# Kernel tuning notes

Measured on AMD Instinct MI355X. Metric: run time of the kernel, lower is better.

## Reference

```python
import jax, jax.numpy as jnp
import numpy as np

EPS = 1e-8

def _layernorm(x, gamma, beta):
    # torch-style: std with Bessel correction (ddof=1), eps added to std
    D = x.shape[-1]
    mean = jnp.mean(x, axis=-1, keepdims=True)
    var = jnp.sum((x - mean) ** 2, axis=-1, keepdims=True) / (D - 1)
    std = jnp.sqrt(var)
    return (x - mean) / (std + EPS) * gamma + beta


def setup_inputs() -> dict:
    key = jax.random.key(0)
    B, T, D, H = 1, 2048, 1024, 16
    Dh = D // H
    ks = jax.random.split(key, 8)
    s = 0.02
    return {
        "x": jax.random.normal(ks[0], (B, T, D), jnp.float32),
        "wq": jax.random.normal(ks[1], (H, D, Dh), jnp.float32) * s,
        "wk": jax.random.normal(ks[2], (H, D, Dh), jnp.float32) * s,
        "wv": jax.random.normal(ks[3], (H, D, Dh), jnp.float32) * s,
        "wo": jax.random.normal(ks[4], (D, D), jnp.float32) * s,
        "bo": jnp.zeros((D,), jnp.float32),
        "ln1_g": jnp.ones((D,), jnp.float32),
        "ln1_b": jnp.zeros((D,), jnp.float32),
        "ln2_g": jnp.ones((D,), jnp.float32),
        "ln2_b": jnp.zeros((D,), jnp.float32),
        "w1": jax.random.normal(ks[5], (D, 4 * D), jnp.float32) * s,
        "b1": jnp.zeros((4 * D,), jnp.float32),
        "w2": jax.random.normal(ks[6], (4 * D, D), jnp.float32) * s,
        "b2": jnp.zeros((D,), jnp.float32),
    }


def reference(x, wq, wk, wv, wo, bo, ln1_g, ln1_b, ln2_g, ln2_b, w1, b1, w2, b2):
    B, T, D = x.shape
    H, _, Dh = wq.shape
    # --- attention sublayer (dropout p used at eval => identity) ---
    h = _layernorm(x, ln1_g, ln1_b)
    q = jnp.einsum('btd,hde->bhte', h, wq)
    k = jnp.einsum('btd,hde->bhte', h, wk)
    v = jnp.einsum('btd,hde->bhte', h, wv)
    scores = jnp.einsum('bhte,bhse->bhts', q, k) / jnp.sqrt(jnp.float32(Dh))
    causal = jnp.triu(jnp.ones((T, T), bool), 1)  # True above diagonal => masked
    scores = jnp.where(causal, -jnp.inf, scores)
    attn = jax.nn.softmax(scores, axis=-1)
    ctx = jnp.einsum('bhts,bhse->bthe', attn, v).reshape(B, T, H * Dh)
    att_out = ctx @ wo + bo
    x = x + att_out
    # --- FFN sublayer ---
    h2 = _layernorm(x, ln2_g, ln2_b)
    ffn = jax.nn.gelu(h2 @ w1 + b1, approximate=False) @ w2 + b2
    return x + ffn
```

## Files before the change

### kernel.cpp

```cpp
#include <hip/hip_runtime.h>
#include <hip/hip_bf16.h>
#include <math.h>

typedef unsigned short bf16u;
typedef __attribute__((ext_vector_type(8))) short short8;
typedef __attribute__((ext_vector_type(4))) float floatx4;

__device__ __forceinline__ float bf2f(bf16u u) {
  union { unsigned int i; float f; } c;
  c.i = ((unsigned int)u) << 16;
  return c.f;
}
__device__ __forceinline__ bf16u f2bf(float f) {
  union { float f; unsigned int i; } c;
  c.f = f;
  unsigned int lsb = (c.i >> 16) & 1u;
  c.i += 0x7fffu + lsb;
  return (bf16u)(c.i >> 16);
}

__device__ __forceinline__ void load_lds16(const void* g, void* l) {
  __builtin_amdgcn_global_load_lds(
      (const __attribute__((address_space(1))) void*)g,
      (__attribute__((address_space(3))) void*)l, 16, 0, 0);
}

__global__ __launch_bounds__(256) void ln_kernel(
    const float* __restrict__ x, bf16u* __restrict__ out,
    const float* __restrict__ gamma, const float* __restrict__ beta) {
  const int row = blockIdx.x;
  const int tid = threadIdx.x;
  const int lane = tid & 63, wave = tid >> 6;
  __shared__ float red[4];
  const float* xr = x + (size_t)row * 1024;
  float v[4];
#pragma unroll
  for (int i = 0; i < 4; i++) v[i] = xr[tid + i * 256];
  float s = v[0] + v[1] + v[2] + v[3];
#pragma unroll
  for (int off = 32; off; off >>= 1) s += __shfl_down(s, off);
  if (lane == 0) red[wave] = s;
  __syncthreads();
  const float mean = (red[0] + red[1] + red[2] + red[3]) * (1.0f / 1024.0f);
  __syncthreads();
  float sq = 0.f;
#pragma unroll
  for (int i = 0; i < 4; i++) { float d = v[i] - mean; sq += d * d; }
#pragma unroll
  for (int off = 32; off; off >>= 1) sq += __shfl_down(sq, off);
  if (lane == 0) red[wave] = sq;
  __syncthreads();
  const float var = (red[0] + red[1] + red[2] + red[3]) * (1.0f / 1023.0f);
  const float inv = 1.0f / (sqrtf(var) + 1e-8f);
  bf16u* orow = out + (size_t)row * 1024;
#pragma unroll
  for (int i = 0; i < 4; i++) {
    int idx = tid + i * 256;
    orow[idx] = f2bf((v[i] - mean) * inv * gamma[idx] + beta[idx]);
  }
}

__global__ __launch_bounds__(256) void pack_weights(
    const float* __restrict__ wq, const float* __restrict__ wk,
    const float* __restrict__ wv, const float* __restrict__ wo,
    const float* __restrict__ w1, const float* __restrict__ w2,
    bf16u* __restrict__ WqkvT, bf16u* __restrict__ woT,
    bf16u* __restrict__ w1T, bf16u* __restrict__ w2T) {
  __shared__ bf16u tile[32][33];
  const int id = blockIdx.x;
  const float* in; bf16u* out; int R, C, bx, by;
  if (id < 3072) {
    int job = id >> 10, rem = id & 1023;
    int head = rem >> 6, t = rem & 63;
    bx = t & 1; by = t >> 1;
    in = (job == 0 ? wq : (job == 1 ? wk : wv)) + head * 65536;
    out = WqkvT + job * 1048576 + head * 65536;
    R = 1024; C = 64;
  } else if (id < 4096) {
    int rem = id - 3072; bx = rem & 31; by = rem >> 5;
    in = wo; out = woT; R = 1024; C = 1024;
  } else if (id < 8192) {
    int rem = id - 4096; bx = rem & 127; by = rem >> 7;
    in = w1; out = w1T; R = 1024; C = 4096;
  } else {
    int rem = id - 8192; bx = rem & 31; by = rem >> 5;
    in = w2; out = w2T; R = 4096; C = 1024;
  }
  const int bc = bx * 32, br = by * 32;
  const int lx = threadIdx.x & 31, ly = threadIdx.x >> 5;
#pragma unroll
  for (int i = 0; i < 32; i += 8)
    tile[ly + i][lx] = f2bf(in[(size_t)(br + ly + i) * C + bc + lx]);
  __syncthreads();
#pragma unroll
  for (int i = 0; i < 32; i += 8)
    out[(size_t)(bc + ly + i) * R + br + lx] = tile[lx][ly + i];
}

__global__ __launch_bounds__(256) void transpose_b(
    const bf16u* __restrict__ in, bf16u* __restrict__ out,
    int ins, int coff, int outs) {
  __shared__ bf16u tile[32][33];
  const int bc = blockIdx.x * 32, br = blockIdx.y * 32;
  const int lx = threadIdx.x & 31, ly = threadIdx.x >> 5;
#pragma unroll
  for (int i = 0; i < 32; i += 8)
    tile[ly + i][lx] = in[(size_t)(br + ly + i) * ins + coff + bc + lx];
  __syncthreads();
#pragma unroll
  for (int i = 0; i < 32; i += 8)
    out[(size_t)(bc + ly + i) * outs + br + lx] = tile[lx][ly + i];
}

template <int BM, int BN, int WGR, int WGC, int EPI>
__global__ __launch_bounds__(256, (BN == 128 ? 2 : 4)) void gemm_bt(
    const bf16u* __restrict__ A, const bf16u* __restrict__ Bt,
    const float* __restrict__ bias, const float* __restrict__ res,
    void* __restrict__ Cout, int M, int N, int K, int kchunk) {
  constexpr int BK = 64;
  constexpr int TM = BM / WGR, TN = BN / WGC;
  constexpr int NI = TM / 16, NJ = TN / 16;
  alignas(16) __shared__ bf16u sA[BM * BK];
  alignas(16) __shared__ bf16u sB[BN * BK];
  const int tid = threadIdx.x, lane = tid & 63, wave = tid >> 6;
  const int wr = wave / WGC, wc = wave % WGC;
  const int quad = lane >> 4, l16 = lane & 15;
  const int m0 = blockIdx.y * BM, n0 = blockIdx.x * BN;
  const int kz = blockIdx.z;
  const int kbeg = kz * kchunk;
  const int kend = (kbeg + kchunk < K) ? (kbeg + kchunk) : K;

  floatx4 acc[NI][NJ] = {};
  constexpr int ACH = BM * BK / 8;
  constexpr int BCH = BN * BK / 8;

  for (int k0 = kbeg; k0 < kend; k0 += BK) {
#pragma unroll
    for (int c = tid; c < ACH; c += 256) {
      int r = c >> 3, kc = ((c ^ r) & 7) * 8;
      load_lds16(A + (size_t)(m0 + r) * K + k0 + kc, (void*)(sA + c * 8));
    }
#pragma unroll
    for (int c = tid; c < BCH; c += 256) {
      int r = c >> 3, kc = ((c ^ r) & 7) * 8;
      load_lds16(Bt + (size_t)(n0 + r) * K + k0 + kc, (void*)(sB + c * 8));
    }
    __syncthreads();
#pragma unroll
    for (int kk = 0; kk < BK; kk += 32) {
      const int ch = (kk >> 3) + quad;
      short8 af[NI], bf[NJ];
#pragma unroll
      for (int i = 0; i < NI; i++) {
        const int R = wr * TM + i * 16 + l16;
        af[i] = *(const short8*)(sA + R * BK + ((ch ^ (R & 7)) << 3));
      }
#pragma unroll
      for (int j = 0; j < NJ; j++) {
        const int R = wc * TN + j * 16 + l16;
        bf[j] = *(const short8*)(sB + R * BK + ((ch ^ (R & 7)) << 3));
      }
#pragma unroll
      for (int i = 0; i < NI; i++)
#pragma unroll
        for (int j = 0; j < NJ; j++)
          acc[i][j] = __builtin_amdgcn_mfma_f32_16x16x32_bf16(af[i], bf[j], acc[i][j], 0, 0, 0);
    }
    __syncthreads();
  }

  float* pout = (float*)Cout;
  if constexpr (EPI == 3) pout += (size_t)kz * M * N;
#pragma unroll
  for (int j = 0; j < NJ; j++) {
    const int col = n0 + wc * TN + j * 16 + l16;
    float bv = 0.0f;
    if constexpr (EPI == 1 || EPI == 2) bv = bias[col];
#pragma unroll
    for (int i = 0; i < NI; i++) {
#pragma unroll
      for (int r = 0; r < 4; r++) {
        const int row = m0 + wr * TM + i * 16 + quad * 4 + r;
        const size_t o = (size_t)row * N + col;
        const float v = acc[i][j][r];
        if constexpr (EPI == 0) {
          ((bf16u*)Cout)[o] = f2bf(v);
        } else if constexpr (EPI == 1) {
          pout[o] = v + bv + res[o];
        } else if constexpr (EPI == 2) {
          float t = v + bv;
          ((bf16u*)Cout)[o] = f2bf(0.5f * t * (1.0f + erff(t * 0.70710678118654752f)));
        } else {
          pout[o] = v;
        }
      }
    }
  }
}

__global__ __launch_bounds__(256) void reduce2_kernel(
    const float* __restrict__ part, const float* __restrict__ bias,
    const float* __restrict__ res, float* __restrict__ out,
    int N, size_t total) {
  size_t i = ((size_t)blockIdx.x * 256 + threadIdx.x) * 4;
  if (i >= total) return;
  float4 a = *(const float4*)(part + i);
  float4 b = *(const float4*)(part + total + i);
  float4 r = *(const float4*)(res + i);
  float4 bv = *(const float4*)(bias + (int)(i & (size_t)(N - 1)));
  float4 o;
  o.x = a.x + b.x + r.x + bv.x;
  o.y = a.y + b.y + r.y + bv.y;
  o.z = a.z + b.z + r.z + bv.z;
  o.w = a.w + b.w + r.w + bv.w;
  *(float4*)(out + i) = o;
}

template <int NT>
__device__ __forceinline__ void attn_tile(
    const bf16u* sQ, const bf16u* sK, const bf16u* sVt, bf16u* sP,
    floatx4* aco, floatx4& acc_l, short8 ones,
    int q0, int c0, int wave, int quad, int l16) {
  constexpr int SK = 72, SV = 136;
  floatx4 s[NT] = {};
#pragma unroll
  for (int kk = 0; kk < 64; kk += 32) {
    short8 aq = *(const short8*)(sQ + (wave * 16 + l16) * SK + kk + quad * 8);
#pragma unroll
    for (int nt = 0; nt < NT; nt++) {
      short8 bk = *(const short8*)(sK + (nt * 16 + l16) * SK + kk + quad * 8);
      s[nt] = __builtin_amdgcn_mfma_f32_16x16x32_bf16(bk, aq, s[nt], 0, 0, 0);
    }
  }
  const float C = 0.125f * 1.44269504088896f;
  const int qrow = q0 + wave * 16 + l16;
#pragma unroll
  for (int nt = 0; nt < NT; nt++)
#pragma unroll
    for (int r = 0; r < 4; r++) {
      const int kpos = c0 + nt * 16 + quad * 4 + r;
      float t = s[nt][r] * C;
      if (kpos > qrow) t = -__builtin_inff();
      s[nt][r] = __builtin_amdgcn_exp2f(t);
    }
  __syncthreads();
#pragma unroll
  for (int nt = 0; nt < NT; nt++) {
    unsigned int lo = (unsigned int)f2bf(s[nt][0]) | ((unsigned int)f2bf(s[nt][1]) << 16);
    unsigned int hi = (unsigned int)f2bf(s[nt][2]) | ((unsigned int)f2bf(s[nt][3]) << 16);
    uint2 pk; pk.x = lo; pk.y = hi;
    *(uint2*)(sP + (wave * 16 + l16) * SV + nt * 16 + quad * 4) = pk;
  }
  __syncthreads();
#pragma unroll
  for (int kk = 0; kk < NT * 16; kk += 32) {
    short8 ap = *(const short8*)(sP + (wave * 16 + l16) * SV + kk + quad * 8);
#pragma unroll
    for (int dt = 0; dt < 4; dt++) {
      short8 bv = *(const short8*)(sVt + (dt * 16 + l16) * SV + kk + quad * 8);
      aco[dt] = __builtin_amdgcn_mfma_f32_16x16x32_bf16(ap, bv, aco[dt], 0, 0, 0);
    }
    acc_l = __builtin_amdgcn_mfma_f32_16x16x32_bf16(ap, ones, acc_l, 0, 0, 0);
  }
}

__global__ __launch_bounds__(256, 3) void flash_attn(
    const bf16u* __restrict__ QKV, const bf16u* __restrict__ Vt,
    bf16u* __restrict__ ctx) {
  const int qb = 31 - blockIdx.x;
  const int h = blockIdx.y;
  const int tid = threadIdx.x, lane = tid & 63, wave = tid >> 6;
  const int quad = lane >> 4, l16 = lane & 15;
  constexpr int SK = 72, SV = 136;
  alignas(16) __shared__ bf16u sQ[64 * SK];
  alignas(16) __shared__ bf16u sK[128 * SK];
  alignas(16) __shared__ bf16u sVt[64 * SV];
  bf16u* sP = sK;
  const int q0 = qb * 64;

  for (int c = tid; c < 512; c += 256) {
    int r = c >> 3, e8 = (c & 7) * 8;
    *(uint4*)(sQ + r * SK + e8) =
        *(const uint4*)(QKV + (size_t)(q0 + r) * 3072 + h * 64 + e8);
  }

  floatx4 acc_l = {0.f, 0.f, 0.f, 0.f};
  floatx4 aco[4] = {};
  short8 ones;
#pragma unroll
  for (int u = 0; u < 8; u++) ones[u] = (short)0x3F80;

  const int nkt = (qb >> 1) + 1;
  for (int kt = 0; kt < nkt; kt++) {
    const int c0 = kt * 128;
    __syncthreads();
    for (int c = tid; c < 1024; c += 256) {
      int r = c >> 3, e8 = (c & 7) * 8;
      *(uint4*)(sK + r * SK + e8) =
          *(const uint4*)(QKV + (size_t)(c0 + r) * 3072 + 1024 + h * 64 + e8);
    }
    for (int c = tid; c < 1024; c += 256) {
      int e = c >> 4, s8 = (c & 15) * 8;
      *(uint4*)(sVt + e * SV + s8) =
          *(const uint4*)(Vt + (size_t)(h * 64 + e) * 2048 + c0 + s8);
    }
    __syncthreads();
    if (kt == nkt - 1 && (qb & 1) == 0)
      attn_tile<4>(sQ, sK, sVt, sP, aco, acc_l, ones, q0, c0, wave, quad, l16);
    else
      attn_tile<8>(sQ, sK, sVt, sP, aco, acc_l, ones, q0, c0, wave, quad, l16);
  }
#pragma unroll
  for (int dt = 0; dt < 4; dt++)
#pragma unroll
    for (int r = 0; r < 4; r++) {
      int t = q0 + wave * 16 + quad * 4 + r;
      ctx[(size_t)t * 1024 + h * 64 + dt * 16 + l16] = f2bf(aco[dt][r] / acc_l[r]);
    }
}

extern "C" void kernel_launch(void* const* d_in, const int* in_sizes, int n_in,
                              void* d_out, int out_size, void* d_ws, size_t ws_size,
                              hipStream_t stream) {
  (void)in_sizes; (void)n_in; (void)out_size; (void)ws_size;
  const float* x   = (const float*)d_in[0];
  const float* wq  = (const float*)d_in[1];
  const float* wk  = (const float*)d_in[2];
  const float* wv  = (const float*)d_in[3];
  const float* wo  = (const float*)d_in[4];
  const float* bo  = (const float*)d_in[5];
  const float* g1  = (const float*)d_in[6];
  const float* be1 = (const float*)d_in[7];
  const float* g2  = (const float*)d_in[8];
  const float* be2 = (const float*)d_in[9];
  const float* w1  = (const float*)d_in[10];
  const float* bb1 = (const float*)d_in[11];
  const float* w2  = (const float*)d_in[12];
  const float* bb2 = (const float*)d_in[13];

  char* p = (char*)d_ws;
  const size_t MB = 1024 * 1024;
  bf16u* WqkvT = (bf16u*)(p + 0 * MB);
  bf16u* woT   = (bf16u*)(p + 6 * MB);
  bf16u* w1T   = (bf16u*)(p + 8 * MB);
  bf16u* w2T   = (bf16u*)(p + 16 * MB);
  bf16u* hln   = (bf16u*)(p + 24 * MB);
  bf16u* QKV   = (bf16u*)(p + 28 * MB);
  bf16u* ctx   = (bf16u*)(p + 40 * MB);
  float* x1    = (float*)(p + 44 * MB);
  bf16u* mid   = (bf16u*)(p + 28 * MB);
  float* part  = (float*)(p + 0 * MB);
  bf16u* Vtr   = hln;
  bf16u* h2    = hln;

  pack_weights<<<12288, 256, 0, stream>>>(wq, wk, wv, wo, w1, w2,
                                          WqkvT, woT, w1T, w2T);

  ln_kernel<<<2048, 256, 0, stream>>>(x, hln, g1, be1);
  gemm_bt<64, 128, 2, 2, 0><<<dim3(24, 32, 1), 256, 0, stream>>>(
      hln, WqkvT, nullptr, nullptr, QKV, 2048, 3072, 1024, 1024);
  transpose_b<<<dim3(32, 64), 256, 0, stream>>>(QKV, Vtr, 3072, 2048, 2048);
  flash_attn<<<dim3(32, 16), 256, 0, stream>>>(QKV, Vtr, ctx);
  gemm_bt<32, 64, 2, 2, 1><<<dim3(16, 64, 1), 256, 0, stream>>>(
      ctx, woT, bo, x, x1, 2048, 1024, 1024, 1024);
  ln_kernel<<<2048, 256, 0, stream>>>(x1, h2, g2, be2);
  gemm_bt<64, 128, 2, 2, 2><<<dim3(32, 32, 1), 256, 0, stream>>>(
      h2, w1T, bb1, nullptr, mid, 2048, 4096, 1024, 1024);
  gemm_bt<64, 64, 2, 2, 3><<<dim3(16, 32, 2), 256, 0, stream>>>(
      mid, w2T, nullptr, nullptr, part, 2048, 1024, 4096, 2048);
  reduce2_kernel<<<2048, 256, 0, stream>>>(part, bb2, x1, (float*)d_out,
                                           1024, (size_t)2048 * 1024);
}
```

Before: 296.8 us.

## Split causal flash attention across key tiles with a separate reduction kernel

The flash attention kernel now takes a grid z-dimension of 4 and each block handles every fourth key tile. It writes unnormalized partial outputs in bf16, plus partial row sums. A new attn_reduce kernel adds the partials and normalizes them into ctx. The aim is more blocks and better balance across the uneven causal workload, at the cost of an extra launch, about 16MB of partial-output traffic, and some bf16 rounding on the partials. Workspace buffers are reassigned so the partials fit.

```diff
diff --git a/kernel.cpp b/kernel.cpp
--- a/kernel.cpp
+++ b/kernel.cpp
@@ -264,11 +264,13 @@
   }
 }
 
+template <int NZ>
 __global__ __launch_bounds__(256, 3) void flash_attn(
     const bf16u* __restrict__ QKV, const bf16u* __restrict__ Vt,
-    bf16u* __restrict__ ctx) {
+    bf16u* __restrict__ partO, float* __restrict__ partL) {
   const int qb = 31 - blockIdx.x;
   const int h = blockIdx.y;
+  const int z = blockIdx.z;
   const int tid = threadIdx.x, lane = tid & 63, wave = tid >> 6;
   const int quad = lane >> 4, l16 = lane & 15;
   constexpr int SK = 72, SV = 136;
@@ -291,7 +293,7 @@
   for (int u = 0; u < 8; u++) ones[u] = (short)0x3F80;
 
   const int nkt = (qb >> 1) + 1;
-  for (int kt = 0; kt < nkt; kt++) {
+  for (int kt = z; kt < nkt; kt += NZ) {
     const int c0 = kt * 128;
     __syncthreads();
     for (int c = tid; c < 1024; c += 256) {
@@ -310,13 +312,41 @@
     else
       attn_tile<8>(sQ, sK, sVt, sP, aco, acc_l, ones, q0, c0, wave, quad, l16);
   }
+  bf16u* po = partO + ((size_t)z * 2048 + q0) * 1024 + h * 64;
 #pragma unroll
   for (int dt = 0; dt < 4; dt++)
 #pragma unroll
-    for (int r = 0; r < 4; r++) {
-      int t = q0 + wave * 16 + quad * 4 + r;
-      ctx[(size_t)t * 1024 + h * 64 + dt * 16 + l16] = f2bf(aco[dt][r] / acc_l[r]);
-    }
+    for (int r = 0; r < 4; r++)
+      po[(wave * 16 + quad * 4 + r) * 1024 + dt * 16 + l16] = f2bf(aco[dt][r]);
+  if (l16 == 0) {
+#pragma unroll
+    for (int r = 0; r < 4; r++)
+      partL[((size_t)z * 2048 + q0 + wave * 16 + quad * 4 + r) * 16 + h] = acc_l[r];
+  }
+}
+
+template <int NZ>
+__global__ __launch_bounds__(256) void attn_reduce(
+    const bf16u* __restrict__ partO, const float* __restrict__ partL,
+    bf16u* __restrict__ ctx) {
+  const int t = blockIdx.x;
+  const int col = threadIdx.x * 4;
+  const int h = col >> 6;
+  float l = 0.f;
+#pragma unroll
+  for (int z = 0; z < NZ; z++) l += partL[((size_t)z * 2048 + t) * 16 + h];
+  float o0 = 0.f, o1 = 0.f, o2 = 0.f, o3 = 0.f;
+#pragma unroll
+  for (int z = 0; z < NZ; z++) {
+    uint2 v = *(const uint2*)(partO + ((size_t)z * 2048 + t) * 1024 + col);
+    o0 += bf2f((bf16u)(v.x & 0xffff)); o1 += bf2f((bf16u)(v.x >> 16));
+    o2 += bf2f((bf16u)(v.y & 0xffff)); o3 += bf2f((bf16u)(v.y >> 16));
+  }
+  const float inv = 1.0f / l;
+  uint2 pk;
+  pk.x = (unsigned int)f2bf(o0 * inv) | ((unsigned int)f2bf(o1 * inv) << 16);
+  pk.y = (unsigned int)f2bf(o2 * inv) | ((unsigned int)f2bf(o3 * inv) << 16);
+  *(uint2*)(ctx + (size_t)t * 1024 + col) = pk;
 }
 
 extern "C" void kernel_launch(void* const* d_in, const int* in_sizes, int n_in,
@@ -340,18 +370,19 @@
 
   char* p = (char*)d_ws;
   const size_t MB = 1024 * 1024;
+  constexpr int NZ = 4;
   bf16u* WqkvT = (bf16u*)(p + 0 * MB);
   bf16u* woT   = (bf16u*)(p + 6 * MB);
   bf16u* w1T   = (bf16u*)(p + 8 * MB);
   bf16u* w2T   = (bf16u*)(p + 16 * MB);
-  bf16u* hln   = (bf16u*)(p + 24 * MB);
+  bf16u* multi = (bf16u*)(p + 24 * MB);
   bf16u* QKV   = (bf16u*)(p + 28 * MB);
-  bf16u* ctx   = (bf16u*)(p + 40 * MB);
-  float* x1    = (float*)(p + 44 * MB);
+  float* partL = (float*)(p + 40 * MB);
+  bf16u* partO = (bf16u*)(p + 41 * MB);
   bf16u* mid   = (bf16u*)(p + 28 * MB);
-  float* part  = (float*)(p + 0 * MB);
-  bf16u* Vtr   = hln;
-  bf16u* h2    = hln;
+  float* x1    = (float*)(p + 49 * MB);
+  float* partF = (float*)(p + 0 * MB);
+  bf16u* hln = multi, *Vtr = multi, *ctx = multi, *h2 = multi;
 
   pack_weights<<<12288, 256, 0, stream>>>(wq, wk, wv, wo, w1, w2,
                                           WqkvT, woT, w1T, w2T);
@@ -360,14 +391,15 @@
   gemm_bt<64, 128, 2, 2, 0><<<dim3(24, 32, 1), 256, 0, stream>>>(
       hln, WqkvT, nullptr, nullptr, QKV, 2048, 3072, 1024, 1024);
   transpose_b<<<dim3(32, 64), 256, 0, stream>>>(QKV, Vtr, 3072, 2048, 2048);
-  flash_attn<<<dim3(32, 16), 256, 0, stream>>>(QKV, Vtr, ctx);
+  flash_attn<NZ><<<dim3(32, 16, NZ), 256, 0, stream>>>(QKV, Vtr, partO, partL);
+  attn_reduce<NZ><<<2048, 256, 0, stream>>>(partO, partL, ctx);
   gemm_bt<32, 64, 2, 2, 1><<<dim3(16, 64, 1), 256, 0, stream>>>(
       ctx, woT, bo, x, x1, 2048, 1024, 1024, 1024);
   ln_kernel<<<2048, 256, 0, stream>>>(x1, h2, g2, be2);
   gemm_bt<64, 128, 2, 2, 2><<<dim3(32, 32, 1), 256, 0, stream>>>(
       h2, w1T, bb1, nullptr, mid, 2048, 4096, 1024, 1024);
   gemm_bt<64, 64, 2, 2, 3><<<dim3(16, 32, 2), 256, 0, stream>>>(
-      mid, w2T, nullptr, nullptr, part, 2048, 1024, 4096, 2048);
-  reduce2_kernel<<<2048, 256, 0, stream>>>(part, bb2, x1, (float*)d_out,
+      mid, w2T, nullptr, nullptr, partF, 2048, 1024, 4096, 2048);
+  reduce2_kernel<<<2048, 256, 0, stream>>>(partF, bb2, x1, (float*)d_out,
                                            1024, (size_t)2048 * 1024);
 }
```

After: 288.6 us. 1.03x faster.
